# Kernel optimization log

Measured on AMD Instinct MI355X. Metric: run time of the kernel, lower is better.

The kernel has to match this reference:

```python
import jax, jax.numpy as jnp
import numpy as np

B, T, E, H = 2, 2048, 768, 12
HD = E // H  # 64


def setup_inputs() -> dict:
    key = jax.random.key(0)
    ks = jax.random.split(key, 5)
    s = 0.02
    return {
        "token_embeddings": jax.random.normal(ks[0], (B, T, E), dtype=jnp.float32),
        "W_Q": jax.random.normal(ks[1], (E, E), dtype=jnp.float32) * s,
        "W_K": jax.random.normal(ks[2], (E, E), dtype=jnp.float32) * s,
        "W_V": jax.random.normal(ks[3], (E, E), dtype=jnp.float32) * s,
        "W_pool": jax.random.normal(ks[4], (E, E), dtype=jnp.float32) * s,
    }


def reference(token_embeddings, W_Q, W_K, W_V, W_pool):
    # torch Linear (bias=False): y = x @ W.T with W of shape (out, in)
    Q = token_embeddings @ W_Q.T
    K = token_embeddings @ W_K.T
    V = token_embeddings @ W_V.T
    # Faithful replication of the module's unusual head split:
    # contiguous view (B, T, E) -> (B, H, T, HD), NOT the standard split+transpose.
    Q = Q.reshape(B, H, T, HD)
    K = K.reshape(B, H, T, HD)
    V = V.reshape(B, H, T, HD)
    scores = jnp.einsum("bhqd,bhkd->bhqk", Q, K)  # [B,H,T,T]
    causal = jnp.tril(jnp.ones((T, T), dtype=bool))
    scores = jnp.where(causal, scores, -jnp.inf)
    attn = jax.nn.softmax(scores / jnp.float32(np.sqrt(HD)), axis=-1)
    out = jnp.einsum("bhqk,bhkd->bhqd", attn, V)  # [B,H,T,HD]
    # Faithful: transpose(1,2) then contiguous view back to (B, T, E)
    out = jnp.transpose(out, (0, 2, 1, 3)).reshape(B, T, E)
    return out @ W_pool.T
```

## Files before the change

### kernel.cpp

```cpp
#include <hip/hip_runtime.h>

typedef unsigned short u16;
typedef __attribute__((ext_vector_type(8))) short bf16x8;
typedef __attribute__((ext_vector_type(4))) float f32x4;
typedef __attribute__((ext_vector_type(4))) unsigned short u16x4;

#define GM 4096
#define GN 768
#define GK 768

static __device__ __forceinline__ u16 f2bf(float f) {
  union { float f; unsigned u; } v; v.f = f;
  unsigned u = v.u;
  return (u16)((u + 0x7FFFu + ((u >> 16) & 1u)) >> 16);
}

static __device__ __forceinline__ void gld16(const void* g, void* l) {
  __builtin_amdgcn_global_load_lds((__attribute__((address_space(1))) void*)(g),
                                   (__attribute__((address_space(3))) void*)(l),
                                   16, 0, 0);
}

__global__ void cvt_bf16(const float* __restrict__ in, u16* __restrict__ out, int n4) {
  int i = blockIdx.x * blockDim.x + threadIdx.x;
  if (i < n4) {
    float4 v = ((const float4*)in)[i];
    u16x4 o;
    o[0] = f2bf(v.x); o[1] = f2bf(v.y); o[2] = f2bf(v.z); o[3] = f2bf(v.w);
    ((u16x4*)out)[i] = o;
  }
}

__global__ void cvt_w4(const float* __restrict__ w0, const float* __restrict__ w1,
                       const float* __restrict__ w2, const float* __restrict__ w3,
                       u16* __restrict__ o0, u16* __restrict__ o1,
                       u16* __restrict__ o2, u16* __restrict__ o3, int n4) {
  const float* in = blockIdx.y == 0 ? w0 : (blockIdx.y == 1 ? w1 : (blockIdx.y == 2 ? w2 : w3));
  u16* out = blockIdx.y == 0 ? o0 : (blockIdx.y == 1 ? o1 : (blockIdx.y == 2 ? o2 : o3));
  int i = blockIdx.x * blockDim.x + threadIdx.x;
  if (i < n4) {
    float4 v = ((const float4*)in)[i];
    u16x4 o;
    o[0] = f2bf(v.x); o[1] = f2bf(v.y); o[2] = f2bf(v.z); o[3] = f2bf(v.w);
    ((u16x4*)out)[i] = o;
  }
}

template<int F32OUT>
static __device__ __forceinline__ void gemm_core(const u16* __restrict__ A,
                                                 const u16* __restrict__ B,
                                                 void* __restrict__ O,
                                                 u16* lA, u16* lB)
{
  const int tid = threadIdx.x;
  const int wave = tid >> 6, lane = tid & 63;
  const int g = lane >> 4, c = lane & 15;
  const int wr = (wave >> 1) * 64, wc = (wave & 1) * 64;
  const int tm = blockIdx.x * 128, tn = blockIdx.y * 128;

  f32x4 acc[4][4] = {};

  const int srow = lane >> 2;
  const int scolb = (lane & 3) * 16;
  const char* gA = (const char*)(A + (size_t)tm * GK);
  const char* gB = (const char*)(B + (size_t)tn * GK);

  for (int k0 = 0; k0 < GK; k0 += 32) {
#pragma unroll
    for (int i = 0; i < 2; ++i) {
      const int chunk = wave * 2 + i;
      const int row = chunk * 16 + srow;
      gld16(gA + (size_t)row * (GK * 2) + k0 * 2 + scolb, (char*)lA + chunk * 1024);
      gld16(gB + (size_t)row * (GK * 2) + k0 * 2 + scolb, (char*)lB + chunk * 1024);
    }
    __syncthreads();
    bf16x8 af[4], bfr[4];
#pragma unroll
    for (int m = 0; m < 4; ++m)
      af[m] = *(const bf16x8*)((const char*)lA + (wr + m * 16 + c) * 64 + g * 16);
#pragma unroll
    for (int n = 0; n < 4; ++n)
      bfr[n] = *(const bf16x8*)((const char*)lB + (wc + n * 16 + c) * 64 + g * 16);
#pragma unroll
    for (int m = 0; m < 4; ++m)
#pragma unroll
      for (int n = 0; n < 4; ++n)
        acc[m][n] = __builtin_amdgcn_mfma_f32_16x16x32_bf16(af[m], bfr[n], acc[m][n], 0, 0, 0);
    __syncthreads();
  }

#pragma unroll
  for (int m = 0; m < 4; ++m)
#pragma unroll
    for (int n = 0; n < 4; ++n) {
      const int row0 = tm + wr + m * 16 + g * 4;
      const int col = tn + wc + n * 16 + c;
#pragma unroll
      for (int r = 0; r < 4; ++r) {
        if (F32OUT)
          ((float*)O)[(size_t)(row0 + r) * GN + col] = acc[m][n][r];
        else
          ((u16*)O)[(size_t)(row0 + r) * GN + col] = f2bf(acc[m][n][r]);
      }
    }
}

__global__ __launch_bounds__(256) void gemm_qkv(const u16* __restrict__ A,
    const u16* __restrict__ B0, const u16* __restrict__ B1, const u16* __restrict__ B2,
    u16* __restrict__ O0, u16* __restrict__ O1, u16* __restrict__ O2)
{
  __shared__ u16 lA[4096], lB[4096];
  const u16* B = blockIdx.z == 0 ? B0 : (blockIdx.z == 1 ? B1 : B2);
  u16* O = blockIdx.z == 0 ? O0 : (blockIdx.z == 1 ? O1 : O2);
  gemm_core<0>(A, B, O, lA, lB);
}

__global__ __launch_bounds__(256) void gemm_pool(const u16* __restrict__ A,
    const u16* __restrict__ B, float* __restrict__ O)
{
  __shared__ u16 lA[4096], lB[4096];
  gemm_core<1>(A, B, O, lA, lB);
}

__global__ __launch_bounds__(256) void vtrans(const u16* __restrict__ V, u16* __restrict__ VT) {
  const int tblk = blockIdx.x;
  const int bh = blockIdx.y;
  __shared__ u16 tile[64][72];
  const u16* Vh = V + (size_t)bh * 131072;
  u16* Vt = VT + (size_t)bh * 131072;
  const int tid = threadIdx.x;
  const int t0 = tblk * 64;
#pragma unroll
  for (int i = 0; i < 4; ++i) {
    int idx = i * 256 + tid;
    int row = idx >> 4;
    int c4 = idx & 15;
    u16x4 v = *(const u16x4*)(Vh + (size_t)(t0 + row) * 64 + c4 * 4);
    tile[row][c4 * 4 + 0] = v[0]; tile[row][c4 * 4 + 1] = v[1];
    tile[row][c4 * 4 + 2] = v[2]; tile[row][c4 * 4 + 3] = v[3];
  }
  __syncthreads();
#pragma unroll
  for (int i = 0; i < 4; ++i) {
    int idx = i * 256 + tid;
    int d = idx >> 4;
    int t4 = idx & 15;
    u16x4 o;
    o[0] = tile[t4 * 4 + 0][d]; o[1] = tile[t4 * 4 + 1][d];
    o[2] = tile[t4 * 4 + 2][d]; o[3] = tile[t4 * 4 + 3][d];
    *(u16x4*)(Vt + (size_t)d * 2048 + t0 + t4 * 4) = o;
  }
}

static __device__ __forceinline__ void stage_tile(const char* gbase, int rowstride,
                                                  char* lbuf, int wave, int lane) {
#pragma unroll
  for (int i = 0; i < 2; ++i) {
    const int chunk = i * 256 + wave * 64 + lane;
    const int row = chunk >> 3;
    const int colb = (chunk & 7) << 4;
    const char* src = gbase + (size_t)row * rowstride + (colb ^ ((row & 7) << 4));
    char* dst = lbuf + i * 4096 + wave * 1024;
    gld16(src, dst);
  }
}

__global__ __launch_bounds__(256, 4) void attn(const u16* __restrict__ Q,
                                               const u16* __restrict__ Km,
                                               const u16* __restrict__ VT,
                                               u16* __restrict__ X2)
{
  const int qblk = blockIdx.x;
  const int bh = blockIdx.y;
  const int b = bh / 12, h = bh % 12;
  const int tid = threadIdx.x, wave = tid >> 6, lane = tid & 63;
  const int g = lane >> 4, c = lane & 15;
  const int swr = (c & 7) << 4;

  __shared__ char Kl[2][8192];
  __shared__ char Vl[2][8192];
  __shared__ u16 Plds[4][1024];
  u16* pl = Plds[wave];

  const char* Khb = (const char*)(Km + (size_t)bh * 131072);
  const char* Vhb = (const char*)(VT + (size_t)bh * 131072);
  const u16* Qh = Q + (size_t)bh * 131072;

  const int q0 = qblk * 64 + wave * 16;
  const int nkt = qblk + 1;

  stage_tile(Khb, 128, Kl[0], wave, lane);
  stage_tile(Vhb, 4096, Vl[0], wave, lane);

  bf16x8 qf[2];
#pragma unroll
  for (int kk = 0; kk < 2; ++kk)
    qf[kk] = *(const bf16x8*)(Qh + (size_t)(q0 + c) * 64 + kk * 32 + g * 8);

  f32x4 oacc[4] = {};
  float lsum[4] = {0.f, 0.f, 0.f, 0.f};

  __syncthreads();

  for (int kt = 0; kt < nkt; ++kt) {
    const int cur = kt & 1;
    if (kt + 1 < nkt) {
      stage_tile(Khb + (size_t)(kt + 1) * 8192, 128, Kl[cur ^ 1], wave, lane);
      stage_tile(Vhb + (size_t)(kt + 1) * 128, 4096, Vl[cur ^ 1], wave, lane);
    }
    f32x4 s[4] = {};
#pragma unroll
    for (int kk = 0; kk < 2; ++kk)
#pragma unroll
      for (int n = 0; n < 4; ++n) {
        bf16x8 kf = *(const bf16x8*)(Kl[cur] + (size_t)(n * 16 + c) * 128 + ((kk * 64 + g * 16) ^ swr));
        s[n] = __builtin_amdgcn_mfma_f32_16x16x32_bf16(qf[kk], kf, s[n], 0, 0, 0);
      }
    if (kt == nkt - 1) {
#pragma unroll
      for (int n = 0; n < 4; ++n) {
        const int key = kt * 64 + n * 16 + c;
#pragma unroll
        for (int r = 0; r < 4; ++r) {
          const int row = g * 4 + r;
          float p = (key > q0 + row) ? 0.f : __expf(s[n][r] * 0.125f);
          lsum[r] += p;
          const int sw = ((row & 7) ^ (row >> 3)) << 4;
          *(u16*)((char*)pl + row * 128 + ((n * 32 + c * 2) ^ sw)) = f2bf(p);
        }
      }
    } else {
#pragma unroll
      for (int n = 0; n < 4; ++n)
#pragma unroll
        for (int r = 0; r < 4; ++r) {
          const int row = g * 4 + r;
          float p = __expf(s[n][r] * 0.125f);
          lsum[r] += p;
          const int sw = ((row & 7) ^ (row >> 3)) << 4;
          *(u16*)((char*)pl + row * 128 + ((n * 32 + c * 2) ^ sw)) = f2bf(p);
        }
    }
#pragma unroll
    for (int kk = 0; kk < 2; ++kk) {
      const int swp = ((c & 7) ^ (c >> 3)) << 4;
      bf16x8 pa = *(const bf16x8*)((const char*)pl + c * 128 + ((kk * 64 + g * 16) ^ swp));
#pragma unroll
      for (int n = 0; n < 4; ++n) {
        bf16x8 vf = *(const bf16x8*)(Vl[cur] + (size_t)(n * 16 + c) * 128 + ((kk * 64 + g * 16) ^ swr));
        oacc[n] = __builtin_amdgcn_mfma_f32_16x16x32_bf16(pa, vf, oacc[n], 0, 0, 0);
      }
    }
    __syncthreads();
  }

  float linv[4];
#pragma unroll
  for (int r = 0; r < 4; ++r) {
    float ps = lsum[r];
    ps += __shfl_xor(ps, 1);
    ps += __shfl_xor(ps, 2);
    ps += __shfl_xor(ps, 4);
    ps += __shfl_xor(ps, 8);
    linv[r] = __frcp_rn(ps);
  }
#pragma unroll
  for (int n = 0; n < 4; ++n)
#pragma unroll
    for (int r = 0; r < 4; ++r) {
      const float o = oacc[n][r] * linv[r];
      const int t = q0 + g * 4 + r;
      X2[((size_t)b * 2048 + t) * 768 + h * 64 + n * 16 + c] = f2bf(o);
    }
}

extern "C" void kernel_launch(void* const* d_in, const int* in_sizes, int n_in,
                              void* d_out, int out_size, void* d_ws, size_t ws_size,
                              hipStream_t stream) {
  const float* x  = (const float*)d_in[0];
  const float* wq = (const float*)d_in[1];
  const float* wk = (const float*)d_in[2];
  const float* wv = (const float*)d_in[3];
  const float* wp = (const float*)d_in[4];

  const size_t SZ_X = (size_t)GM * GN * 2;
  const size_t SZ_W = (size_t)GK * GN * 2;
  char* ws = (char*)d_ws;
  u16* xbf  = (u16*)(ws);
  u16* wqb  = (u16*)(ws + SZ_X);
  u16* wkb  = (u16*)(ws + SZ_X + SZ_W);
  u16* wvb  = (u16*)(ws + SZ_X + 2 * SZ_W);
  u16* wpb  = (u16*)(ws + SZ_X + 3 * SZ_W);
  u16* Qb   = (u16*)(ws + SZ_X + 4 * SZ_W);
  u16* Kb   = (u16*)(ws + 2 * SZ_X + 4 * SZ_W);
  u16* Vb   = (u16*)(ws + 3 * SZ_X + 4 * SZ_W);
  u16* VT   = (u16*)(ws + 4 * SZ_X + 4 * SZ_W);
  u16* X2   = (u16*)(ws + 5 * SZ_X + 4 * SZ_W);
  if (ws_size < 6 * SZ_X + 4 * SZ_W) return;

  cvt_bf16<<<dim3(3072), dim3(256), 0, stream>>>(x, xbf, GM * GN / 4);
  cvt_w4<<<dim3(576, 4), dim3(256), 0, stream>>>(wq, wk, wv, wp, wqb, wkb, wvb, wpb, GK * GN / 4);

  gemm_qkv<<<dim3(32, 6, 3), dim3(256), 0, stream>>>(xbf, wqb, wkb, wvb, Qb, Kb, Vb);
  vtrans<<<dim3(32, 24), dim3(256), 0, stream>>>(Vb, VT);
  attn<<<dim3(32, 24), dim3(256), 0, stream>>>(Qb, Kb, VT, X2);
  gemm_pool<<<dim3(32, 6), dim3(256), 0, stream>>>(X2, wpb, (float*)d_out);
}
```

Before: 110.4 us.

## Schedule causal attention tiles longest-first via atomic work queue; transpose score layout

The attention kernel now pulls work items from a global atomic counter and processes query blocks in descending order of causal length, so the longest tiles start first and load balances across CUs. The QK MFMA operands are swapped so each lane holds four consecutive keys for one query row. That lets P be written to LDS as packed 8-byte stores and cuts the row-sum reduction to fewer shuffles. It also adds s_setprio around the MFMA sections. The queue costs an extra memset and an atomic plus barrier per item, and a stale counter would break correctness if the memset were skipped.

```diff
diff --git a/kernel.cpp b/kernel.cpp
--- a/kernel.cpp
+++ b/kernel.cpp
@@ -1,18 +1,25 @@
 #include <hip/hip_runtime.h>
 
 typedef unsigned short u16;
+typedef unsigned int u32;
 typedef __attribute__((ext_vector_type(8))) short bf16x8;
 typedef __attribute__((ext_vector_type(4))) float f32x4;
 typedef __attribute__((ext_vector_type(4))) unsigned short u16x4;
+typedef __attribute__((ext_vector_type(2))) unsigned int u32x2;
 
 #define GM 4096
 #define GN 768
 #define GK 768
+#define NITEMS 768
 
 static __device__ __forceinline__ u16 f2bf(float f) {
   union { float f; unsigned u; } v; v.f = f;
   unsigned u = v.u;
   return (u16)((u + 0x7FFFu + ((u >> 16) & 1u)) >> 16);
+}
+
+static __device__ __forceinline__ u32 pack_bf16(float lo, float hi) {
+  return (u32)f2bf(lo) | ((u32)f2bf(hi) << 16);
 }
 
 static __device__ __forceinline__ void gld16(const void* g, void* l) {
@@ -168,110 +175,120 @@
 __global__ __launch_bounds__(256, 4) void attn(const u16* __restrict__ Q,
                                                const u16* __restrict__ Km,
                                                const u16* __restrict__ VT,
-                                               u16* __restrict__ X2)
+                                               u16* __restrict__ X2,
+                                               u32* __restrict__ qcount)
 {
-  const int qblk = blockIdx.x;
-  const int bh = blockIdx.y;
-  const int b = bh / 12, h = bh % 12;
   const int tid = threadIdx.x, wave = tid >> 6, lane = tid & 63;
   const int g = lane >> 4, c = lane & 15;
   const int swr = (c & 7) << 4;
+  const int swz = ((c & 7) ^ (c >> 3)) << 4;
 
   __shared__ char Kl[2][8192];
   __shared__ char Vl[2][8192];
   __shared__ u16 Plds[4][1024];
+  __shared__ int s_item;
   u16* pl = Plds[wave];
 
-  const char* Khb = (const char*)(Km + (size_t)bh * 131072);
-  const char* Vhb = (const char*)(VT + (size_t)bh * 131072);
-  const u16* Qh = Q + (size_t)bh * 131072;
-
-  const int q0 = qblk * 64 + wave * 16;
-  const int nkt = qblk + 1;
-
-  stage_tile(Khb, 128, Kl[0], wave, lane);
-  stage_tile(Vhb, 4096, Vl[0], wave, lane);
-
-  bf16x8 qf[2];
-#pragma unroll
-  for (int kk = 0; kk < 2; ++kk)
-    qf[kk] = *(const bf16x8*)(Qh + (size_t)(q0 + c) * 64 + kk * 32 + g * 8);
-
-  f32x4 oacc[4] = {};
-  float lsum[4] = {0.f, 0.f, 0.f, 0.f};
-
-  __syncthreads();
-
-  for (int kt = 0; kt < nkt; ++kt) {
-    const int cur = kt & 1;
-    if (kt + 1 < nkt) {
-      stage_tile(Khb + (size_t)(kt + 1) * 8192, 128, Kl[cur ^ 1], wave, lane);
-      stage_tile(Vhb + (size_t)(kt + 1) * 128, 4096, Vl[cur ^ 1], wave, lane);
+  for (;;) {
+    if (tid == 0) s_item = (int)atomicAdd(qcount, 1u);
+    __syncthreads();
+    const int w = s_item;
+    if (w >= NITEMS) return;
+    const int qblk = 31 - (w / 24);
+    const int bh = w % 24;
+    const int b = bh / 12, h = bh % 12;
+
+    const char* Khb = (const char*)(Km + (size_t)bh * 131072);
+    const char* Vhb = (const char*)(VT + (size_t)bh * 131072);
+    const u16* Qh = Q + (size_t)bh * 131072;
+
+    const int q0 = qblk * 64 + wave * 16;
+    const int nkt = qblk + 1;
+
+    stage_tile(Khb, 128, Kl[0], wave, lane);
+    stage_tile(Vhb, 4096, Vl[0], wave, lane);
+
+    bf16x8 qf[2];
+#pragma unroll
+    for (int kk = 0; kk < 2; ++kk)
+      qf[kk] = *(const bf16x8*)(Qh + (size_t)(q0 + c) * 64 + kk * 32 + g * 8);
+
+    f32x4 oacc[4] = {};
+    float lsum = 0.f;
+
+    __syncthreads();
+
+    for (int kt = 0; kt < nkt; ++kt) {
+      const int cur = kt & 1;
+      if (kt + 1 < nkt) {
+        stage_tile(Khb + (size_t)(kt + 1) * 8192, 128, Kl[cur ^ 1], wave, lane);
+        stage_tile(Vhb + (size_t)(kt + 1) * 128, 4096, Vl[cur ^ 1], wave, lane);
+      }
+      f32x4 s[4] = {};
+      __builtin_amdgcn_s_setprio(1);
+#pragma unroll
+      for (int kk = 0; kk < 2; ++kk)
+#pragma unroll
+        for (int n = 0; n < 4; ++n) {
+          bf16x8 kf = *(const bf16x8*)(Kl[cur] + (size_t)(n * 16 + c) * 128 + ((kk * 64 + g * 16) ^ swr));
+          s[n] = __builtin_amdgcn_mfma_f32_16x16x32_bf16(kf, qf[kk], s[n], 0, 0, 0);
+        }
+      __builtin_amdgcn_s_setprio(0);
+      if (kt == nkt - 1) {
+        const int qrow = q0 + c;
+#pragma unroll
+        for (int n = 0; n < 4; ++n) {
+          const int k0i = kt * 64 + n * 16 + g * 4;
+          float p0 = (k0i + 0 > qrow) ? 0.f : __expf(s[n][0] * 0.125f);
+          float p1 = (k0i + 1 > qrow) ? 0.f : __expf(s[n][1] * 0.125f);
+          float p2 = (k0i + 2 > qrow) ? 0.f : __expf(s[n][2] * 0.125f);
+          float p3 = (k0i + 3 > qrow) ? 0.f : __expf(s[n][3] * 0.125f);
+          lsum += (p0 + p1) + (p2 + p3);
+          u32x2 pw; pw[0] = pack_bf16(p0, p1); pw[1] = pack_bf16(p2, p3);
+          *(u32x2*)((char*)pl + c * 128 + ((n * 32 + g * 8) ^ swz)) = pw;
+        }
+      } else {
+#pragma unroll
+        for (int n = 0; n < 4; ++n) {
+          float p0 = __expf(s[n][0] * 0.125f);
+          float p1 = __expf(s[n][1] * 0.125f);
+          float p2 = __expf(s[n][2] * 0.125f);
+          float p3 = __expf(s[n][3] * 0.125f);
+          lsum += (p0 + p1) + (p2 + p3);
+          u32x2 pw; pw[0] = pack_bf16(p0, p1); pw[1] = pack_bf16(p2, p3);
+          *(u32x2*)((char*)pl + c * 128 + ((n * 32 + g * 8) ^ swz)) = pw;
+        }
+      }
+      __builtin_amdgcn_s_setprio(1);
+#pragma unroll
+      for (int kk = 0; kk < 2; ++kk) {
+        bf16x8 pa = *(const bf16x8*)((const char*)pl + c * 128 + ((kk * 64 + g * 16) ^ swz));
+#pragma unroll
+        for (int n = 0; n < 4; ++n) {
+          bf16x8 vf = *(const bf16x8*)(Vl[cur] + (size_t)(n * 16 + c) * 128 + ((kk * 64 + g * 16) ^ swr));
+          oacc[n] = __builtin_amdgcn_mfma_f32_16x16x32_bf16(pa, vf, oacc[n], 0, 0, 0);
+        }
+      }
+      __builtin_amdgcn_s_setprio(0);
+      __syncthreads();
     }
-    f32x4 s[4] = {};
-#pragma unroll
-    for (int kk = 0; kk < 2; ++kk)
-#pragma unroll
-      for (int n = 0; n < 4; ++n) {
-        bf16x8 kf = *(const bf16x8*)(Kl[cur] + (size_t)(n * 16 + c) * 128 + ((kk * 64 + g * 16) ^ swr));
-        s[n] = __builtin_amdgcn_mfma_f32_16x16x32_bf16(qf[kk], kf, s[n], 0, 0, 0);
-      }
-    if (kt == nkt - 1) {
-#pragma unroll
-      for (int n = 0; n < 4; ++n) {
-        const int key = kt * 64 + n * 16 + c;
-#pragma unroll
-        for (int r = 0; r < 4; ++r) {
-          const int row = g * 4 + r;
-          float p = (key > q0 + row) ? 0.f : __expf(s[n][r] * 0.125f);
-          lsum[r] += p;
-          const int sw = ((row & 7) ^ (row >> 3)) << 4;
-          *(u16*)((char*)pl + row * 128 + ((n * 32 + c * 2) ^ sw)) = f2bf(p);
-        }
-      }
-    } else {
-#pragma unroll
-      for (int n = 0; n < 4; ++n)
-#pragma unroll
-        for (int r = 0; r < 4; ++r) {
-          const int row = g * 4 + r;
-          float p = __expf(s[n][r] * 0.125f);
-          lsum[r] += p;
-          const int sw = ((row & 7) ^ (row >> 3)) << 4;
-          *(u16*)((char*)pl + row * 128 + ((n * 32 + c * 2) ^ sw)) = f2bf(p);
-        }
-    }
-#pragma unroll
-    for (int kk = 0; kk < 2; ++kk) {
-      const int swp = ((c & 7) ^ (c >> 3)) << 4;
-      bf16x8 pa = *(const bf16x8*)((const char*)pl + c * 128 + ((kk * 64 + g * 16) ^ swp));
-#pragma unroll
-      for (int n = 0; n < 4; ++n) {
-        bf16x8 vf = *(const bf16x8*)(Vl[cur] + (size_t)(n * 16 + c) * 128 + ((kk * 64 + g * 16) ^ swr));
-        oacc[n] = __builtin_amdgcn_mfma_f32_16x16x32_bf16(pa, vf, oacc[n], 0, 0, 0);
-      }
-    }
-    __syncthreads();
-  }
-
-  float linv[4];
-#pragma unroll
-  for (int r = 0; r < 4; ++r) {
-    float ps = lsum[r];
-    ps += __shfl_xor(ps, 1);
-    ps += __shfl_xor(ps, 2);
-    ps += __shfl_xor(ps, 4);
-    ps += __shfl_xor(ps, 8);
-    linv[r] = __frcp_rn(ps);
-  }
-#pragma unroll
-  for (int n = 0; n < 4; ++n)
-#pragma unroll
-    for (int r = 0; r < 4; ++r) {
-      const float o = oacc[n][r] * linv[r];
-      const int t = q0 + g * 4 + r;
-      X2[((size_t)b * 2048 + t) * 768 + h * 64 + n * 16 + c] = f2bf(o);
-    }
+
+    float tot = lsum;
+    tot += __shfl_xor(tot, 16);
+    tot += __shfl_xor(tot, 32);
+    float linv[4];
+#pragma unroll
+    for (int r = 0; r < 4; ++r)
+      linv[r] = __frcp_rn(__shfl(tot, g * 4 + r));
+#pragma unroll
+    for (int n = 0; n < 4; ++n)
+#pragma unroll
+      for (int r = 0; r < 4; ++r) {
+        const float o = oacc[n][r] * linv[r];
+        const int t = q0 + g * 4 + r;
+        X2[((size_t)b * 2048 + t) * 768 + h * 64 + n * 16 + c] = f2bf(o);
+      }
+  }
 }
 
 extern "C" void kernel_launch(void* const* d_in, const int* in_sizes, int n_in,
@@ -296,13 +313,15 @@
   u16* Vb   = (u16*)(ws + 3 * SZ_X + 4 * SZ_W);
   u16* VT   = (u16*)(ws + 4 * SZ_X + 4 * SZ_W);
   u16* X2   = (u16*)(ws + 5 * SZ_X + 4 * SZ_W);
-  if (ws_size < 6 * SZ_X + 4 * SZ_W) return;
+  u32* qcount = (u32*)(ws + 6 * SZ_X + 4 * SZ_W);
+  if (ws_size < 6 * SZ_X + 4 * SZ_W + 256) return;
 
   cvt_bf16<<<dim3(3072), dim3(256), 0, stream>>>(x, xbf, GM * GN / 4);
   cvt_w4<<<dim3(576, 4), dim3(256), 0, stream>>>(wq, wk, wv, wp, wqb, wkb, wvb, wpb, GK * GN / 4);
+  hipMemsetAsync(qcount, 0, sizeof(u32), stream);
 
   gemm_qkv<<<dim3(32, 6, 3), dim3(256), 0, stream>>>(xbf, wqb, wkb, wvb, Qb, Kb, Vb);
   vtrans<<<dim3(32, 24), dim3(256), 0, stream>>>(Vb, VT);
-  attn<<<dim3(32, 24), dim3(256), 0, stream>>>(Qb, Kb, VT, X2);
+  attn<<<dim3(768), dim3(256), 0, stream>>>(Qb, Kb, VT, X2, qcount);
   gemm_pool<<<dim3(32, 6), dim3(256), 0, stream>>>(X2, wpb, (float*)d_out);
 }
```

New measurement: 109.0 us. Within noise of the previous version (-1.2%).
